# Kernel tuning notes

Measured on AMD Instinct MI355X. Metric: run time of the kernel, lower is better.

Reference implementation:

```python
import jax, jax.numpy as jnp
import numpy as np

ARITY = 4  # matches init_kwargs; params.shape[1] == 2**ARITY


def _high_order_act(X, params):
    # X: [B, G*arity], params: [G, 2**arity, O]
    B = X.shape[0]
    G, _, O = params.shape
    a = ARITY
    A = X.reshape(B, G, a)
    # sort ascending along the arity dim (torch.sort returns values + indices)
    A_ind = jnp.argsort(A, axis=2)                      # [B, G, a] int32
    A_sort = jnp.take_along_axis(A, A_ind, axis=2)      # [B, G, a]
    # barycentric-style coefficients: smallest value, then successive diffs
    coef = jnp.concatenate(
        [A_sort[:, :, :1], A_sort[:, :, 1:] - A_sort[:, :, :-1]], axis=2
    )                                                   # [B, G, a]
    # bit-power index: reverse cumsum of 2**A_ind -> suffix sums of bit masks
    pow2 = jnp.left_shift(jnp.int32(1), A_ind.astype(jnp.int32))  # [B, G, a]
    idx = jnp.cumsum(pow2[:, :, ::-1], axis=2)[:, :, ::-1]        # [B, G, a], in [1, 2**a - 1]
    # gather per-group table rows: params[g, idx[b,g,k], :]
    g_idx = jnp.arange(G)[None, :, None]                # [1, G, 1]
    gathered = params[g_idx, idx]                       # [B, G, a, O]
    # einsum 'jikl,ijk->ijl' in torch (j=G, i=B) == 'bgao,bga->bgo' here
    out = jnp.einsum('bgao,bga->bgo', gathered, coef)   # [B, G, O]
    return out.reshape(B, G * O)


def setup_inputs() -> dict:
    key = jax.random.key(0)
    kx, kp = jax.random.split(key)
    B, G, a, O = 8192, 256, ARITY, 16
    X = jax.random.normal(kx, (B, G * a), dtype=jnp.float32)
    params = jax.random.normal(kp, (G, 2 ** a, O), dtype=jnp.float32)
    return {"X": X, "params": params}


def reference(X, params):
    return _high_order_act(X, params)
```

## Files before the change

### kernel.cpp

```cpp
#include <hip/hip_runtime.h>


#define TB 16
#define TG 16
#define TSTRIDE 260

__global__ __launch_bounds__(256) void hoa_kernel(
    const float* __restrict__ X, const float* __restrict__ P,
    float* __restrict__ out, int B, int G)
{
    __shared__ float lds[TG * TSTRIDE];

    const int tid = threadIdx.x;
    const int g0 = blockIdx.y * TG;
    const int b0 = blockIdx.x * TB;

    #pragma unroll
    for (int i = 0; i < (TG * 64) / 256; ++i) {
        int ci = tid + i * 256;
        int table = ci >> 6;
        int within = ci & 63;
        float4 v = *reinterpret_cast<const float4*>(
            P + (size_t)(g0 + table) * 256 + within * 4);
        *reinterpret_cast<float4*>(&lds[table * TSTRIDE + within * 4]) = v;
    }
    __syncthreads();

    const int gg = tid & (TG - 1);
    const int bb = tid >> 4;
    const int b  = b0 + bb;
    const int g  = g0 + gg;
    if (b >= B) return;

    float4 x = *reinterpret_cast<const float4*>(X + (size_t)b * (G * 4) + g * 4);
    float v0 = x.x, v1 = x.y, v2 = x.z, v3 = x.w;
    int i0 = 0, i1 = 1, i2 = 2, i3 = 3;

#define CSWAP(va, vb, ia, ib)                         \
    {                                                 \
        bool sw_ = (va) > (vb);                       \
        float lo_ = sw_ ? (vb) : (va);                \
        float hi_ = sw_ ? (va) : (vb);                \
        int il_ = sw_ ? (ib) : (ia);                  \
        int ih_ = sw_ ? (ia) : (ib);                  \
        (va) = lo_; (vb) = hi_; (ia) = il_; (ib) = ih_; \
    }
    CSWAP(v0, v1, i0, i1);
    CSWAP(v2, v3, i2, i3);
    CSWAP(v0, v2, i0, i2);
    CSWAP(v1, v3, i1, i3);
    CSWAP(v1, v2, i1, i2);
#undef CSWAP

    float c0 = v0, c1 = v1 - v0, c2 = v2 - v1, c3 = v3 - v2;
    int p0 = 1 << i0, p1 = 1 << i1, p3 = 1 << i3;
    int idx0 = 15;
    int idx1 = 15 ^ p0;
    int idx2 = idx1 ^ p1;
    int idx3 = p3;

    const float* tab = &lds[gg * TSTRIDE];
    const float4* r0 = reinterpret_cast<const float4*>(tab + idx0 * 16);
    const float4* r1 = reinterpret_cast<const float4*>(tab + idx1 * 16);
    const float4* r2 = reinterpret_cast<const float4*>(tab + idx2 * 16);
    const float4* r3 = reinterpret_cast<const float4*>(tab + idx3 * 16);

    float* ob = out + (size_t)b * (G * 16) + g * 16;
    #pragma unroll
    for (int c = 0; c < 4; ++c) {
        float4 A = r0[c], Bv = r1[c], C = r2[c], D = r3[c];
        float4 o;
        o.x = fmaf(c3, D.x, fmaf(c2, C.x, fmaf(c1, Bv.x, c0 * A.x)));
        o.y = fmaf(c3, D.y, fmaf(c2, C.y, fmaf(c1, Bv.y, c0 * A.y)));
        o.z = fmaf(c3, D.z, fmaf(c2, C.z, fmaf(c1, Bv.z, c0 * A.z)));
        o.w = fmaf(c3, D.w, fmaf(c2, C.w, fmaf(c1, Bv.w, c0 * A.w)));
        reinterpret_cast<float4*>(ob)[c] = o;
    }
}

extern "C" void kernel_launch(void* const* d_in, const int* in_sizes, int n_in,
                              void* d_out, int out_size, void* d_ws, size_t ws_size,
                              hipStream_t stream) {
    const float* X = (const float*)d_in[0];
    const float* P = (const float*)d_in[1];
    float* out = (float*)d_out;

    int G = in_sizes[1] / 256;
    int B = in_sizes[0] / (G * 4);

    dim3 grid((B + TB - 1) / TB, G / TG);
    hipLaunchKernelGGL(hoa_kernel, grid, dim3(256), 0, stream, X, P, out, B, G);
}
```

Baseline: 179.9 us.

## Split each output row across four threads for coalesced float4 stores

Each (b,g) pair is now handled by four threads, each computing and storing one float4 of the 16 outputs, and the block size grows to 1024. Consecutive lanes then write contiguous memory, which is meant to improve store coalescing on the large output. The cost is redundant X loads and sort work per thread, plus larger blocks that may reduce scheduling flexibility.

```diff
diff --git a/kernel.cpp b/kernel.cpp
--- a/kernel.cpp
+++ b/kernel.cpp
@@ -5,7 +5,7 @@
 #define TG 16
 #define TSTRIDE 260
 
-__global__ __launch_bounds__(256) void hoa_kernel(
+__global__ __launch_bounds__(1024) void hoa_kernel(
     const float* __restrict__ X, const float* __restrict__ P,
     float* __restrict__ out, int B, int G)
 {
@@ -15,19 +15,18 @@
     const int g0 = blockIdx.y * TG;
     const int b0 = blockIdx.x * TB;
 
-    #pragma unroll
-    for (int i = 0; i < (TG * 64) / 256; ++i) {
-        int ci = tid + i * 256;
-        int table = ci >> 6;
-        int within = ci & 63;
+    {
+        int table = tid >> 6;
+        int within = tid & 63;
         float4 v = *reinterpret_cast<const float4*>(
             P + (size_t)(g0 + table) * 256 + within * 4);
         *reinterpret_cast<float4*>(&lds[table * TSTRIDE + within * 4]) = v;
     }
     __syncthreads();
 
-    const int gg = tid & (TG - 1);
-    const int bb = tid >> 4;
+    const int c  = tid & 3;
+    const int gg = (tid >> 2) & 15;
+    const int bb = tid >> 6;
     const int b  = b0 + bb;
     const int g  = g0 + gg;
     if (b >= B) return;
@@ -53,29 +52,24 @@
 #undef CSWAP
 
     float c0 = v0, c1 = v1 - v0, c2 = v2 - v1, c3 = v3 - v2;
-    int p0 = 1 << i0, p1 = 1 << i1, p3 = 1 << i3;
     int idx0 = 15;
-    int idx1 = 15 ^ p0;
-    int idx2 = idx1 ^ p1;
-    int idx3 = p3;
+    int idx1 = 15 ^ (1 << i0);
+    int idx2 = idx1 ^ (1 << i1);
+    int idx3 = 1 << i3;
 
-    const float* tab = &lds[gg * TSTRIDE];
-    const float4* r0 = reinterpret_cast<const float4*>(tab + idx0 * 16);
-    const float4* r1 = reinterpret_cast<const float4*>(tab + idx1 * 16);
-    const float4* r2 = reinterpret_cast<const float4*>(tab + idx2 * 16);
-    const float4* r3 = reinterpret_cast<const float4*>(tab + idx3 * 16);
+    const float* tab = &lds[gg * TSTRIDE + c * 4];
+    float4 A  = *reinterpret_cast<const float4*>(tab + idx0 * 16);
+    float4 Bv = *reinterpret_cast<const float4*>(tab + idx1 * 16);
+    float4 C  = *reinterpret_cast<const float4*>(tab + idx2 * 16);
+    float4 D  = *reinterpret_cast<const float4*>(tab + idx3 * 16);
 
-    float* ob = out + (size_t)b * (G * 16) + g * 16;
-    #pragma unroll
-    for (int c = 0; c < 4; ++c) {
-        float4 A = r0[c], Bv = r1[c], C = r2[c], D = r3[c];
-        float4 o;
-        o.x = fmaf(c3, D.x, fmaf(c2, C.x, fmaf(c1, Bv.x, c0 * A.x)));
-        o.y = fmaf(c3, D.y, fmaf(c2, C.y, fmaf(c1, Bv.y, c0 * A.y)));
-        o.z = fmaf(c3, D.z, fmaf(c2, C.z, fmaf(c1, Bv.z, c0 * A.z)));
-        o.w = fmaf(c3, D.w, fmaf(c2, C.w, fmaf(c1, Bv.w, c0 * A.w)));
-        reinterpret_cast<float4*>(ob)[c] = o;
-    }
+    float4 o;
+    o.x = fmaf(c3, D.x, fmaf(c2, C.x, fmaf(c1, Bv.x, c0 * A.x)));
+    o.y = fmaf(c3, D.y, fmaf(c2, C.y, fmaf(c1, Bv.y, c0 * A.y)));
+    o.z = fmaf(c3, D.z, fmaf(c2, C.z, fmaf(c1, Bv.z, c0 * A.z)));
+    o.w = fmaf(c3, D.w, fmaf(c2, C.w, fmaf(c1, Bv.w, c0 * A.w)));
+
+    *reinterpret_cast<float4*>(out + (size_t)b * (G * 16) + g * 16 + c * 4) = o;
 }
 
 extern "C" void kernel_launch(void* const* d_in, const int* in_sizes, int n_in,
@@ -89,5 +83,5 @@
     int B = in_sizes[0] / (G * 4);
 
     dim3 grid((B + TB - 1) / TB, G / TG);
-    hipLaunchKernelGGL(hoa_kernel, grid, dim3(256), 0, stream, X, P, out, B, G);
+    hipLaunchKernelGGL(hoa_kernel, grid, dim3(1024), 0, stream, X, P, out, B, G);
 }
```

After: 176.2 us. -2.0%, faster.
